# Performance work log

Measured on AMD Instinct MI355X. Metric: run time of the kernel, lower is better.

The kernel has to match this reference:

```python
import jax, jax.numpy as jnp
import numpy as np

L, D, H, F = 6, 1024, 8, 2048
B, S, IN = 4, 2048, 128
DK = D // H
EPS = 1e-6


def layer_norm(x, s, b):
    mu = jnp.mean(x, -1, keepdims=True)
    var = jnp.mean((x - mu) ** 2, -1, keepdims=True)
    return (x - mu) * jax.lax.rsqrt(var + EPS) * s + b


def rotate_every_two(x):
    x1 = x[..., ::2]
    x2 = x[..., 1::2]
    return jnp.stack([-x2, x1], axis=-1).reshape(x.shape)


def rotary_tables():
    # torchscale RetNet xpos-style angles: each freq repeated twice (interleaved)
    angle = 1.0 / (10000.0 ** jnp.linspace(0.0, 1.0, DK // 2))
    angle = jnp.repeat(angle, 2)                      # [DK]
    idx = jnp.arange(S, dtype=jnp.float32)[:, None]   # [S,1]
    return jnp.sin(idx * angle), jnp.cos(idx * angle)  # [S,DK] each


def decay_mask():
    # gamma_h = 1 - 2^(-5-h); D[h,n,m] = gamma_h^(n-m) for n>=m else 0,
    # row-normalized by sqrt(row sum) as in torchscale.
    gamma = 1.0 - 2.0 ** (-5.0 - jnp.arange(H, dtype=jnp.float32))  # [H]
    n = jnp.arange(S)
    diff = jnp.clip(n[:, None] - n[None, :], 0)                      # [S,S]
    tril = n[:, None] >= n[None, :]
    m = jnp.where(tril[None], gamma[:, None, None] ** diff[None].astype(jnp.float32), 0.0)
    return m / jnp.sqrt(jnp.sum(m, -1, keepdims=True))               # [H,S,S]


def setup_inputs() -> dict:
    key = jax.random.key(0)
    ks = iter(jax.random.split(key, 24))
    p = lambda shape: jax.random.normal(next(ks), shape, jnp.float32) * 0.02
    return {
        "x": jax.random.normal(next(ks), (B, S, IN), jnp.float32),
        "W_in": p((IN, D)), "b_in": jnp.zeros((D,), jnp.float32),
        "Wq": p((L, D, D)), "Wk": p((L, D, D)), "Wv": p((L, D, D)),
        "Wg": p((L, D, D)), "Wo": p((L, D, D)),
        "gn_g": jnp.ones((L, D), jnp.float32),
        "ln1_s": jnp.ones((L, D), jnp.float32), "ln1_b": jnp.zeros((L, D), jnp.float32),
        "ffn_W1": p((L, D, F)), "ffn_b1": jnp.zeros((L, F), jnp.float32),
        "ffn_W2": p((L, F, D)), "ffn_b2": jnp.zeros((L, D), jnp.float32),
        "ln2_s": jnp.ones((L, D), jnp.float32), "ln2_b": jnp.zeros((L, D), jnp.float32),
        "lnf_s": jnp.ones((D,), jnp.float32), "lnf_b": jnp.zeros((D,), jnp.float32),
        "W_reg": p((D, 1)), "b_reg": jnp.zeros((1,), jnp.float32),
    }


def reference(x, W_in, b_in, Wq, Wk, Wv, Wg, Wo, gn_g, ln1_s, ln1_b,
              ffn_W1, ffn_b1, ffn_W2, ffn_b2, ln2_s, ln2_b, lnf_s, lnf_b,
              W_reg, b_reg):
    sin, cos = rotary_tables()
    dmask = decay_mask()  # [H,S,S]
    h = x @ W_in + b_in   # input_embed
    for l in range(L):
        # --- multi-scale retention (pre-norm) ---
        y = layer_norm(h, ln1_s[l], ln1_b[l])
        q = (y @ Wq[l]).reshape(B, S, H, DK).transpose(0, 2, 1, 3)
        k = (y @ Wk[l]).reshape(B, S, H, DK).transpose(0, 2, 1, 3) * (DK ** -0.5)
        v = (y @ Wv[l]).reshape(B, S, H, DK).transpose(0, 2, 1, 3)
        q = q * cos + rotate_every_two(q) * sin
        k = k * cos + rotate_every_two(k) * sin
        scores = jnp.einsum('bhnd,bhmd->bhnm', q, k)
        ret = scores * dmask[None]
        ret = ret / jnp.clip(jnp.abs(ret).sum(-1, keepdims=True), 1.0, None)
        o = jnp.einsum('bhnm,bhmd->bhnd', ret, v)
        # per-head group (RMS) norm
        o = o * jax.lax.rsqrt(jnp.mean(o * o, -1, keepdims=True) + EPS)
        o = o.transpose(0, 2, 1, 3).reshape(B, S, D) * gn_g[l]
        g = y @ Wg[l]
        h = h + (jax.nn.silu(g) * o) @ Wo[l]
        # --- FFN (pre-norm) ---
        y = layer_norm(h, ln2_s[l], ln2_b[l])
        h = h + jax.nn.gelu(y @ ffn_W1[l] + ffn_b1[l]) @ ffn_W2[l] + ffn_b2[l]
    h = layer_norm(h, lnf_s, lnf_b)
    out = 1.1 * jax.nn.sigmoid(h @ W_reg + b_reg) - 0.05
    return out.squeeze(-1)  # [B,S]
```

## Files before the change

### kernel.cpp

```cpp
#include <hip/hip_runtime.h>

#define L_ 6
#define D_ 1024
#define H_ 8
#define F_ 2048
#define B_ 4
#define S_ 2048
#define IN_ 128
#define DK_ 128
#define BS_ (B_*S_)
#define D2_ 4096

typedef short bf16x8 __attribute__((ext_vector_type(8)));
typedef float f32x4 __attribute__((ext_vector_type(4)));

__device__ inline float b2f(unsigned short u){ union{unsigned int i; float f;} v; v.i = ((unsigned int)u)<<16; return v.f; }
__device__ inline unsigned short f2b(float f){ union{unsigned int i; float f;} v; v.f = f; unsigned int r = v.i + 0x7FFFu + ((v.i>>16)&1u); return (unsigned short)(r>>16); }
__device__ inline unsigned int cvtpk(float lo, float hi){
    unsigned int r; asm("v_cvt_pk_bf16_f32 %0, %1, %2" : "=v"(r) : "v"(lo), "v"(hi)); return r;
}

__device__ inline void gld16(const void* g, void* l) {
    __builtin_amdgcn_global_load_lds((const __attribute__((address_space(1))) unsigned int*)g,
                                     (__attribute__((address_space(3))) unsigned int*)l, 16, 0, 0);
}

#define GBAR() do{ asm volatile("" ::: "memory"); __builtin_amdgcn_s_barrier(); asm volatile("" ::: "memory"); }while(0)

__global__ void f32_to_bf16_k(const float* __restrict__ in, unsigned short* __restrict__ out, int n)
{
    int i = blockIdx.x*256 + threadIdx.x;
    if (i < n) out[i] = f2b(in[i]);
}

__global__ void transpose_w_k(const float* __restrict__ in, unsigned short* __restrict__ out, int R, int C, size_t ostride)
{
    __shared__ float tile[32][33];
    int z = blockIdx.z;
    const float* pi = in + (size_t)z*R*C;
    unsigned short* po = out + (size_t)z*ostride;
    int c0 = blockIdx.x*32, r0 = blockIdx.y*32;
    int tx = threadIdx.x, ty = threadIdx.y;
    #pragma unroll
    for (int i=0;i<4;i++) tile[ty+i*8][tx] = pi[(size_t)(r0+ty+i*8)*C + c0+tx];
    __syncthreads();
    #pragma unroll
    for (int i=0;i<4;i++) po[(size_t)(c0+ty+i*8)*R + r0+tx] = f2b(tile[tx][ty+i*8]);
}

__global__ void transpose_v_k(const unsigned short* __restrict__ vb, unsigned short* __restrict__ vT)
{
    __shared__ unsigned short tile[32][33];
    int z = blockIdx.z;
    int b = z >> 3, hh = z & 7;
    int s0 = blockIdx.x*32, d0 = blockIdx.y*32;
    int tx = threadIdx.x, ty = threadIdx.y;
    #pragma unroll
    for (int i=0;i<4;i++) tile[ty+i*8][tx] = vb[(size_t)(b*S_ + s0+ty+i*8)*D2_ + hh*DK_ + d0+tx];
    __syncthreads();
    #pragma unroll
    for (int i=0;i<4;i++) vT[((size_t)z*DK_ + d0+ty+i*8)*S_ + s0+tx] = tile[tx][ty+i*8];
}

__global__ void build_sincos_k(float* __restrict__ cost, float* __restrict__ sint)
{
    int id = blockIdx.x*256 + threadIdx.x;
    int s = id >> 6, i = id & 63;
    float ang = powf(10000.f, -(float)i/63.f);
    float a = (float)s * ang;
    float sv = sinf(a), cv = cosf(a);
    sint[s*DK_ + 2*i] = sv; sint[s*DK_ + 2*i+1] = sv;
    cost[s*DK_ + 2*i] = cv; cost[s*DK_ + 2*i+1] = cv;
}

__global__ void build_dnorm_k(float* __restrict__ dnorm)
{
    int id = blockIdx.x*256 + threadIdx.x;
    int h = id >> 11, n = id & (S_-1);
    double g = 1.0 - exp2((double)(-5 - h));
    double sum = (1.0 - exp(((double)(n+1))*log(g))) / (1.0 - g);
    dnorm[id] = (float)(1.0/sqrt(sum));
}

__device__ inline float bsum(float v, float* red, int t)
{
    #pragma unroll
    for (int m=32; m; m>>=1) v += __shfl_xor(v, m);
    __syncthreads();
    if ((t & 63) == 0) red[t>>6] = v;
    __syncthreads();
    return red[0]+red[1]+red[2]+red[3];
}

__global__ __launch_bounds__(256) void ln_to_bf16_k(const float* __restrict__ x, const float* __restrict__ s,
                                                    const float* __restrict__ b, unsigned short* __restrict__ y)
{
    __shared__ float red[4];
    int row = blockIdx.x, t = threadIdx.x;
    const float* xr = x + (size_t)row * D_;
    float4 v = ((const float4*)xr)[t];
    float mu = bsum(v.x+v.y+v.z+v.w, red, t) * (1.f/D_);
    float d0=v.x-mu, d1=v.y-mu, d2=v.z-mu, d3=v.w-mu;
    float var = bsum(d0*d0+d1*d1+d2*d2+d3*d3, red, t) * (1.f/D_);
    float inv = rsqrtf(var + 1e-6f);
    int c = t*4;
    float o0 = d0*inv*s[c+0] + b[c+0];
    float o1 = d1*inv*s[c+1] + b[c+1];
    float o2 = d2*inv*s[c+2] + b[c+2];
    float o3 = d3*inv*s[c+3] + b[c+3];
    unsigned long long pk = (unsigned long long)f2b(o0) | ((unsigned long long)f2b(o1)<<16)
                          | ((unsigned long long)f2b(o2)<<32) | ((unsigned long long)f2b(o3)<<48);
    *(unsigned long long*)(y + (size_t)row*D_ + c) = pk;
}

template<int MODE, int BN>
__global__ __launch_bounds__(512, 2)
void gemm6(const unsigned short* __restrict__ A,
           const unsigned short* __restrict__ Bt,
           const float* __restrict__ bias,
           void* __restrict__ Cv,
           int M, int N, int K)
{
    constexpr int BM   = 256;
    constexpr int IR   = 8;
    constexpr int JR   = BN/64;
    constexpr int ASUB = BM*64;
    constexpr int BSUB = BN*64;
    constexpr int BUFSZ= 2*ASUB + 2*BSUB;
    constexpr int AP   = 2;
    constexpr int BP   = BN/128;
    __shared__ unsigned char lds[2*BUFSZ];

    const int tid = threadIdx.x, lane = tid & 63, w = tid >> 6;
    const int r16 = lane & 15, quad = (lane >> 4) & 3;
    const int wm = w >> 2, wn = w & 3;

    const int nwg = (int)(gridDim.x * gridDim.y);
    int bid = (int)(blockIdx.y * gridDim.x + blockIdx.x);
    if ((nwg & 7) == 0) bid = (bid & 7) * (nwg >> 3) + (bid >> 3);
    const int m0 = (bid / (int)gridDim.x) * BM;
    const int n0 = (bid % (int)gridDim.x) * BN;

    const int srow = tid >> 2;
    const int schk = (tid & 3) ^ ((tid >> 3) & 3);
    const unsigned short* gA = A  + (size_t)(m0 + srow) * K + schk*8;
    const unsigned short* gB = Bt + (size_t)(n0 + srow) * K + schk*8;

    const int rchk = (quad ^ ((r16 >> 1) & 3)) * 16;
    const int aoff = (wm*128 + r16)*64 + rchk;
    const int boff = (wn*(BN/4) + r16)*64 + rchk;

    f32x4 acc[IR][JR];
    #pragma unroll
    for (int i=0;i<IR;i++)
      #pragma unroll
      for (int j=0;j<JR;j++) acc[i][j] = (f32x4){0.f,0.f,0.f,0.f};

    const int NT = K >> 6;

    auto stageA = [&](int t, int kk){
        unsigned char* dst = lds + (t&1)*BUFSZ + kk*ASUB;
        const unsigned short* src = gA + (size_t)t*64 + kk*32;
        #pragma unroll
        for (int p=0;p<AP;p++)
            gld16(src + (size_t)(p*128)*K, dst + p*8192 + tid*16);
    };
    auto stageB = [&](int t, int kk){
        unsigned char* dst = lds + (t&1)*BUFSZ + 2*ASUB + kk*BSUB;
        const unsigned short* src = gB + (size_t)t*64 + kk*32;
        #pragma unroll
        for (int p=0;p<BP;p++)
            gld16(src + (size_t)(p*128)*K, dst + p*8192 + tid*16);
    };

    stageA(0,0); stageB(0,0); stageA(0,1); stageB(0,1);
    if constexpr (BN==256) asm volatile("s_waitcnt vmcnt(4)" ::: "memory");
    else                   asm volatile("s_waitcnt vmcnt(3)" ::: "memory");
    GBAR();

    for (int t = 0; t < NT; ++t) {
        const unsigned char* cb = lds + (t&1)*BUFSZ;
        const bool pre = (t+1 < NT);
        #pragma unroll
        for (int kk = 0; kk < 2; ++kk) {
            const unsigned char* ak = cb + kk*ASUB;
            const unsigned char* bk = cb + 2*ASUB + kk*BSUB;
            if constexpr (BN == 256) {
                bf16x8 af[4], bg[JR];
                #pragma unroll
                for (int i=0;i<4;i++) af[i] = *(const bf16x8*)(ak + aoff + i*1024);
                #pragma unroll
                for (int j=0;j<JR;j++) bg[j] = *(const bf16x8*)(bk + boff + j*1024);
                if (pre) stageA(t+1, kk);
                GBAR();
                asm volatile("s_waitcnt lgkmcnt(0)" ::: "memory");
                __builtin_amdgcn_s_setprio(1);
                #pragma unroll
                for (int i=0;i<4;i++)
                  #pragma unroll
                  for (int j=0;j<JR;j++)
                    acc[i][j] = __builtin_amdgcn_mfma_f32_16x16x32_bf16(af[i], bg[j], acc[i][j], 0,0,0);
                __builtin_amdgcn_s_setprio(0);
                GBAR();
                #pragma unroll
                for (int i=0;i<4;i++) af[i] = *(const bf16x8*)(ak + aoff + (4+i)*1024);
                if (pre) stageB(t+1, kk);
                GBAR();
                asm volatile("s_waitcnt lgkmcnt(0)" ::: "memory");
                __builtin_amdgcn_s_setprio(1);
                #pragma unroll
                for (int i=0;i<4;i++)
                  #pragma unroll
                  for (int j=0;j<JR;j++)
                    acc[4+i][j] = __builtin_amdgcn_mfma_f32_16x16x32_bf16(af[i], bg[j], acc[4+i][j], 0,0,0);
                __builtin_amdgcn_s_setprio(0);
                if (pre) asm volatile("s_waitcnt vmcnt(4)" ::: "memory");
                else     asm volatile("s_waitcnt vmcnt(0)" ::: "memory");
                GBAR();
            } else {
                bf16x8 af[8], bg[JR];
                #pragma unroll
                for (int i=0;i<8;i++) af[i] = *(const bf16x8*)(ak + aoff + i*1024);
                #pragma unroll
                for (int j=0;j<JR;j++) bg[j] = *(const bf16x8*)(bk + boff + j*1024);
                if (pre) { stageA(t+1, kk); stageB(t+1, kk); }
                GBAR();
                asm volatile("s_waitcnt lgkmcnt(0)" ::: "memory");
                __builtin_amdgcn_s_setprio(1);
                #pragma unroll
                for (int i=0;i<8;i++)
                  #pragma unroll
                  for (int j=0;j<JR;j++)
                    acc[i][j] = __builtin_amdgcn_mfma_f32_16x16x32_bf16(af[i], bg[j], acc[i][j], 0,0,0);
                __builtin_amdgcn_s_setprio(0);
                if (pre) asm volatile("s_waitcnt vmcnt(3)" ::: "memory");
                else     asm volatile("s_waitcnt vmcnt(0)" ::: "memory");
                GBAR();
            }
        }
    }

    float* Cf = (float*)Cv;
    unsigned short* Cb = (unsigned short*)Cv;
    float bvs[JR];
    #pragma unroll
    for (int j=0;j<JR;j++) bvs[j] = bias ? bias[n0 + wn*(BN/4) + j*16 + r16] : 0.f;
    #pragma unroll
    for (int i=0;i<IR;i++) {
      #pragma unroll
      for (int r=0;r<4;r++) {
        const size_t crow = (size_t)(m0 + wm*128 + i*16 + quad*4 + r);
        #pragma unroll
        for (int j=0;j<JR;j++) {
          const int ccol = n0 + wn*(BN/4) + j*16 + r16;
          float v = acc[i][j][r];
          if (MODE == 0) { Cf[crow*N + ccol] = v + bvs[j]; }
          else if (MODE == 1) { Cf[crow*N + ccol] += v + bvs[j]; }
          else if (MODE == 2) { Cb[crow*N + ccol] = f2b(v); }
          else {
            v += bvs[j];
            float t3 = tanhf(0.7978845608028654f*(v + 0.044715f*v*v*v));
            Cb[crow*N + ccol] = f2b(0.5f*v*(1.f + t3));
          }
        }
      }
    }
}

__global__ __launch_bounds__(256) void rope_qk_k(unsigned short* __restrict__ qkvg,
                                                 const float* __restrict__ cost, const float* __restrict__ sint)
{
    int id = blockIdx.x*256 + threadIdx.x;
    int row = id >> 9;
    int d = (id & 511) * 2;
    int s = row & (S_-1);
    int dk = d & (DK_-1);
    float c0 = cost[s*DK_ + dk],   s0 = sint[s*DK_ + dk];
    float c1 = cost[s*DK_ + dk+1], s1 = sint[s*DK_ + dk+1];
    size_t off = (size_t)row*D2_ + d;
    unsigned int qu = *(unsigned int*)(qkvg + off);
    float q0 = b2f((unsigned short)(qu & 0xffffu)), q1 = b2f((unsigned short)(qu >> 16));
    float r0 = q0*c0 - q1*s0;
    float r1 = q1*c1 + q0*s1;
    *(unsigned int*)(qkvg + off) = (unsigned int)f2b(r0) | ((unsigned int)f2b(r1) << 16);
    const float sc = 0.08838834764831845f;
    unsigned int ku = *(unsigned int*)(qkvg + off + 1024);
    float k0 = b2f((unsigned short)(ku & 0xffffu))*sc, k1 = b2f((unsigned short)(ku >> 16))*sc;
    float t0 = k0*c0 - k1*s0;
    float t1 = k1*c1 + k0*s1;
    *(unsigned int*)(qkvg + off + 1024) = (unsigned int)f2b(t0) | ((unsigned int)f2b(t1) << 16);
}

__global__ __launch_bounds__(256, 2) void retention_k(const unsigned short* __restrict__ qk_base,
    const unsigned short* __restrict__ vT, const float* __restrict__ dnorm,
    const float* __restrict__ gng, unsigned short* __restrict__ attnin)
{
    __shared__ __align__(16) unsigned char lds[75776];
    const int pr = blockIdx.x;
    const int bh = blockIdx.y;
    const int b = bh >> 3, hh = bh & 7;
    const int tid = threadIdx.x, lane = tid & 63, w = tid >> 6;
    const int r16 = lane & 15, quad = lane >> 4;

    const float l2g = log2f(1.f - exp2f(-5.f - (float)hh));
    const int ithr = (int)(45.f / (-l2g));
    const unsigned int mkr = (r16 & 7) << 4;

    const int mk2  = ((tid >> 4) & 7) << 4;
    const int mkv2 = ((tid >> 3) & 7) << 4;
    const unsigned short* ksrc = qk_base + 1024 + ((size_t)(b*S_) + (tid>>4))*D2_ + hh*DK_
                                + ((((tid&15)*16) ^ mk2) >> 1);
    const unsigned short* vsrc = vT + ((size_t)bh*DK_ + (tid>>3))*S_ + ((((tid&7)*16) ^ mkv2) >> 1);

    float Aarr[4];
    #pragma unroll
    for (int r=0;r<4;r++) Aarr[r] = exp2f(l2g * (float)(63 - (w*16 + quad*4 + r)));

    float* dsums = (float*)(lds + 73728);
    float* ssums = (float*)(lds + 74752);

    auto stage = [&](int c2, int kt2){
        const unsigned short* s0 = ksrc + (size_t)kt2*64*D2_;
        #pragma unroll
        for (int i=0;i<4;i++)
            gld16(s0 + (size_t)i*16*D2_, lds + c2*16384 + i*4096 + w*1024);
        const unsigned short* s1 = vsrc + kt2*64;
        #pragma unroll
        for (int j=0;j<4;j++)
            gld16(s1 + (size_t)j*32*S_, lds + 32768 + c2*16384 + j*4096 + w*1024);
    };

    int cur = 0;

    #pragma unroll 1
    for (int seg = 0; seg < 2; ++seg) {
        const int qt = seg ? pr : (31 - pr);
        const int n0 = qt * 64;
        const int kt_start = max(0, (n0 - ithr) >> 6);

        bf16x8 qf[4][4];
        const unsigned short* qptr = qk_base + ((size_t)(b*S_ + n0 + r16))*D2_ + hh*DK_;
        #pragma unroll
        for (int qtl=0;qtl<4;qtl++)
          #pragma unroll
          for (int c=0;c<4;c++) qf[qtl][c] = *(const bf16x8*)(qptr + qtl*16*D2_ + c*32 + quad*8);

        f32x4 oacc[4][2];
        #pragma unroll
        for (int qtl=0;qtl<4;qtl++)
          #pragma unroll
          for (int dt=0;dt<2;dt++) oacc[qtl][dt] = (f32x4){0.f,0.f,0.f,0.f};
        float dsum[4] = {0.f,0.f,0.f,0.f};

        stage(cur, kt_start);

        #pragma unroll 1
        for (int kt = kt_start; kt <= qt; ++kt) {
            if (kt < qt) { stage(cur^1, kt+1); asm volatile("s_waitcnt vmcnt(8)" ::: "memory"); }
            else         { asm volatile("s_waitcnt vmcnt(0)" ::: "memory"); }
            GBAR();

            const unsigned char* kb = lds + cur*16384;
            bf16x8 kf[4];
            #pragma unroll
            for (int c=0;c<4;c++)
                kf[c] = *(const bf16x8*)(kb + (w*16 + r16)*256 + ((c*64 + quad*16) ^ mkr));
            f32x4 sf[4];
            #pragma unroll
            for (int qtl=0;qtl<4;qtl++) sf[qtl] = (f32x4){0.f,0.f,0.f,0.f};
            __builtin_amdgcn_s_setprio(1);
            #pragma unroll
            for (int c=0;c<4;c++)
              #pragma unroll
              for (int qtl=0;qtl<4;qtl++)
                sf[qtl] = __builtin_amdgcn_mfma_f32_16x16x32_bf16(kf[c], qf[qtl][c], sf[qtl], 0,0,0);
            __builtin_amdgcn_s_setprio(0);

            const bool diag = (kt == qt);
            #pragma unroll
            for (int qtl=0;qtl<4;qtl++) {
                float Bq = exp2f(l2g * (float)(n0 + qtl*16 + r16 - kt*64 - 63));
                float pv[4];
                #pragma unroll
                for (int r=0;r<4;r++) {
                    float p = sf[qtl][r] * Aarr[r] * Bq;
                    if (diag && (w*16 + quad*4 + r > qtl*16 + r16)) p = 0.f;
                    dsum[qtl] += fabsf(p);
                    pv[r] = p;
                }
                unsigned long long pk = (unsigned long long)cvtpk(pv[0], pv[1])
                                      | ((unsigned long long)cvtpk(pv[2], pv[3]) << 32);
                *(unsigned long long*)(lds + 65536 + (qtl*16 + r16)*128 + ((w*32 + quad*8) ^ mkr)) = pk;
            }
            asm volatile("s_waitcnt lgkmcnt(0)" ::: "memory");
            GBAR();

            const unsigned char* vb = lds + 32768 + cur*16384;
            bf16x8 pa[4][2], vf[2][2];
            #pragma unroll
            for (int qtl=0;qtl<4;qtl++)
              #pragma unroll
              for (int ks=0;ks<2;ks++)
                pa[qtl][ks] = *(const bf16x8*)(lds + 65536 + (qtl*16 + r16)*128 + ((ks*64 + quad*16) ^ mkr));
            #pragma unroll
            for (int dt=0;dt<2;dt++)
              #pragma unroll
              for (int ks=0;ks<2;ks++)
                vf[dt][ks] = *(const bf16x8*)(vb + (w*32 + dt*16 + r16)*128 + ((ks*64 + quad*16) ^ mkr));
            __builtin_amdgcn_s_setprio(1);
            #pragma unroll
            for (int qtl=0;qtl<4;qtl++)
              #pragma unroll
              for (int dt=0;dt<2;dt++)
                #pragma unroll
                for (int ks=0;ks<2;ks++)
                  oacc[qtl][dt] = __builtin_amdgcn_mfma_f32_16x16x32_bf16(pa[qtl][ks], vf[dt][ks], oacc[qtl][dt], 0,0,0);
            __builtin_amdgcn_s_setprio(0);
            GBAR();
            cur ^= 1;
        }

        #pragma unroll
        for (int qtl=0;qtl<4;qtl++) {
            float dv = dsum[qtl];
            dv += __shfl_xor(dv, 16); dv += __shfl_xor(dv, 32);
            if (lane < 16) dsums[w*64 + qtl*16 + r16] = dv;
        }
        __syncthreads();
        float scl[4][4], pss[4][4];
        #pragma unroll
        for (int qtl=0;qtl<4;qtl++) {
            #pragma unroll
            for (int r=0;r<4;r++) {
                int nl = qtl*16 + quad*4 + r;
                float dv = dsums[nl] + dsums[64+nl] + dsums[128+nl] + dsums[192+nl];
                float nr = dnorm[hh*S_ + n0 + nl];
                float sc = nr / fmaxf(1.f, dv * nr);
                scl[qtl][r] = sc;
                float s2 = 0.f;
                #pragma unroll
                for (int dt=0;dt<2;dt++) { float t = oacc[qtl][dt][r]*sc; s2 += t*t; }
                s2 += __shfl_xor(s2,1); s2 += __shfl_xor(s2,2);
                s2 += __shfl_xor(s2,4); s2 += __shfl_xor(s2,8);
                pss[qtl][r] = s2;
            }
        }
        if (r16 == 0) {
            #pragma unroll
            for (int qtl=0;qtl<4;qtl++)
              #pragma unroll
              for (int r=0;r<4;r++)
                ssums[w*64 + qtl*16 + quad*4 + r] = pss[qtl][r];
        }
        __syncthreads();
        #pragma unroll
        for (int qtl=0;qtl<4;qtl++) {
            float rms[4];
            #pragma unroll
            for (int r=0;r<4;r++) {
                int nl = qtl*16 + quad*4 + r;
                float s2 = ssums[nl] + ssums[64+nl] + ssums[128+nl] + ssums[192+nl];
                rms[r] = rsqrtf(s2*(1.f/DK_) + 1e-6f);
            }
            #pragma unroll
            for (int dt=0;dt<2;dt++) {
                int d = w*32 + dt*16 + r16;
                float gg = gng[hh*DK_ + d];
                #pragma unroll
                for (int r=0;r<4;r++) {
                    int n = n0 + qtl*16 + quad*4 + r;
                    float gv = b2f(qk_base[(size_t)(b*S_ + n)*D2_ + 3072 + hh*DK_ + d]);
                    float sg = gv / (1.f + expf(-gv));
                    float ov = oacc[qtl][dt][r]*scl[qtl][r]*rms[r]*gg;
                    attnin[(size_t)(b*S_ + n)*D_ + hh*DK_ + d] = f2b(ov*sg);
                }
            }
        }
        __syncthreads();
    }
}

__global__ __launch_bounds__(256) void head_out_k(const float* __restrict__ h, const float* __restrict__ s,
    const float* __restrict__ b, const float* __restrict__ wreg, const float* __restrict__ breg,
    float* __restrict__ out)
{
    __shared__ float red[4];
    int row = blockIdx.x, t = threadIdx.x;
    const float* xr = h + (size_t)row*D_;
    float4 v = ((const float4*)xr)[t];
    float mu = bsum(v.x+v.y+v.z+v.w, red, t) * (1.f/D_);
    float d0=v.x-mu, d1=v.y-mu, d2=v.z-mu, d3=v.w-mu;
    float var = bsum(d0*d0+d1*d1+d2*d2+d3*d3, red, t) * (1.f/D_);
    float inv = rsqrtf(var + 1e-6f);
    int c = t*4;
    float dot = (d0*inv*s[c+0]+b[c+0])*wreg[c+0] + (d1*inv*s[c+1]+b[c+1])*wreg[c+1]
              + (d2*inv*s[c+2]+b[c+2])*wreg[c+2] + (d3*inv*s[c+3]+b[c+3])*wreg[c+3];
    dot = bsum(dot, red, t);
    if (t == 0) out[row] = 1.1f / (1.f + expf(-(dot + breg[0]))) - 0.05f;
}

extern "C" void kernel_launch(void* const* d_in, const int* in_sizes, int n_in,
                              void* d_out, int out_size, void* d_ws, size_t ws_size,
                              hipStream_t stream)
{
    (void)in_sizes; (void)n_in; (void)out_size; (void)ws_size;
    const float* x    = (const float*)d_in[0];
    const float* W_in = (const float*)d_in[1];
    const float* b_in = (const float*)d_in[2];
    const float* Wq   = (const float*)d_in[3];
    const float* Wk   = (const float*)d_in[4];
    const float* Wv   = (const float*)d_in[5];
    const float* Wg   = (const float*)d_in[6];
    const float* Wo   = (const float*)d_in[7];
    const float* gn_g = (const float*)d_in[8];
    const float* ln1s = (const float*)d_in[9];
    const float* ln1b = (const float*)d_in[10];
    const float* W1   = (const float*)d_in[11];
    const float* b1   = (const float*)d_in[12];
    const float* W2   = (const float*)d_in[13];
    const float* b2   = (const float*)d_in[14];
    const float* ln2s = (const float*)d_in[15];
    const float* ln2b = (const float*)d_in[16];
    const float* lnfs = (const float*)d_in[17];
    const float* lnfb = (const float*)d_in[18];
    const float* Wreg = (const float*)d_in[19];
    const float* breg = (const float*)d_in[20];

    char* ws = (char*)d_ws;
    size_t off = 0;
    auto alloc = [&](size_t bytes) { char* p = ws + off; off += (bytes + 255) & ~(size_t)255; return p; };

    const size_t DD = (size_t)D_*D_;
    unsigned short* wqkvgT = (unsigned short*)alloc((size_t)L_*4*DD*2);
    unsigned short* woT  = (unsigned short*)alloc((size_t)L_*DD*2);
    unsigned short* w1T  = (unsigned short*)alloc((size_t)L_*D_*F_*2);
    unsigned short* w2T  = (unsigned short*)alloc((size_t)L_*D_*F_*2);
    unsigned short* winT = (unsigned short*)alloc((size_t)D_*IN_*2);
    unsigned short* x_bf = (unsigned short*)alloc((size_t)BS_*IN_*2);
    float*          hbuf = (float*)alloc((size_t)BS_*D_*4);
    unsigned short* y_bf = (unsigned short*)alloc((size_t)BS_*D_*2);
    unsigned short* qkvg = (unsigned short*)alloc((size_t)BS_*D2_*2);
    unsigned short* vTb  = (unsigned short*)alloc((size_t)BS_*D_*2);
    float*          cost = (float*)alloc((size_t)S_*DK_*4);
    float*          sint = (float*)alloc((size_t)S_*DK_*4);
    float*          dnrm = (float*)alloc((size_t)H_*S_*4);
    unsigned short* attn = y_bf;
    unsigned short* midb = qkvg;

    dim3 tb(32, 8);

    f32_to_bf16_k<<<(BS_*IN_)/256, 256, 0, stream>>>(x, x_bf, BS_*IN_);
    transpose_w_k<<<dim3(32,32,L_), tb, 0, stream>>>(Wq, wqkvgT + 0*DD, D_, D_, 4*DD);
    transpose_w_k<<<dim3(32,32,L_), tb, 0, stream>>>(Wk, wqkvgT + 1*DD, D_, D_, 4*DD);
    transpose_w_k<<<dim3(32,32,L_), tb, 0, stream>>>(Wv, wqkvgT + 2*DD, D_, D_, 4*DD);
    transpose_w_k<<<dim3(32,32,L_), tb, 0, stream>>>(Wg, wqkvgT + 3*DD, D_, D_, 4*DD);
    transpose_w_k<<<dim3(32,32,L_), tb, 0, stream>>>(Wo, woT, D_, D_, DD);
    transpose_w_k<<<dim3(64,32,L_), tb, 0, stream>>>(W1, w1T, D_, F_, (size_t)D_*F_);
    transpose_w_k<<<dim3(32,64,L_), tb, 0, stream>>>(W2, w2T, F_, D_, (size_t)D_*F_);
    transpose_w_k<<<dim3(32, 4, 1), tb, 0, stream>>>(W_in, winT, IN_, D_, (size_t)D_*IN_);
    build_sincos_k<<<(S_*64)/256, 256, 0, stream>>>(cost, sint);
    build_dnorm_k<<<(H_*S_)/256, 256, 0, stream>>>(dnrm);

    gemm6<0,128><<<dim3(D_/128, BS_/256), 512, 0, stream>>>(x_bf, winT, b_in, hbuf, BS_, D_, IN_);

    for (int l = 0; l < L_; ++l) {
        ln_to_bf16_k<<<BS_, 256, 0, stream>>>(hbuf, ln1s + l*D_, ln1b + l*D_, y_bf);
        gemm6<2,256><<<dim3(D2_/256, BS_/256), 512, 0, stream>>>(y_bf, wqkvgT + (size_t)l*4*DD, nullptr, qkvg, BS_, D2_, D_);
        rope_qk_k<<<(BS_*D_/2)/256, 256, 0, stream>>>(qkvg, cost, sint);
        transpose_v_k<<<dim3(S_/32, DK_/32, B_*H_), tb, 0, stream>>>(qkvg + 2048, vTb);
        retention_k<<<dim3(16, B_*H_), 256, 0, stream>>>(qkvg, vTb, dnrm, gn_g + l*D_, attn);
        gemm6<1,128><<<dim3(D_/128, BS_/256), 512, 0, stream>>>(attn, woT + (size_t)l*DD, nullptr, hbuf, BS_, D_, D_);
        ln_to_bf16_k<<<BS_, 256, 0, stream>>>(hbuf, ln2s + l*D_, ln2b + l*D_, y_bf);
        gemm6<3,256><<<dim3(F_/256, BS_/256), 512, 0, stream>>>(y_bf, w1T + (size_t)l*D_*F_, b1 + l*F_, midb, BS_, F_, D_);
        gemm6<1,128><<<dim3(D_/128, BS_/256), 512, 0, stream>>>(midb, w2T + (size_t)l*D_*F_, b2 + l*D_, hbuf, BS_, D_, F_);
    }

    head_out_k<<<BS_, 256, 0, stream>>>(hbuf, lnfs, lnfb, Wreg, breg, (float*)d_out);
}
```

Measured before the change: 2.022 ms.

## Fuse RoPE into QKVG GEMM epilogue and remap retention block order

Removes the separate rope_qk_k pass by applying the rotary embedding and the k scaling inside the QKVG GEMM epilogue. Pair partners are fetched with a lane shuffle, and sin/cos values are read from the tables per output element. This saves one read-modify-write pass over the q and k halves of the QKVG buffer per layer. Separately, the retention kernel's block index is remapped so that consecutive blocks interleave (batch, head) pairs, which likely aims at better load balance or cache locality across the differing decay lengths. The risk is more epilogue cost in the GEMM: a divergent branch and extra table loads.

```diff
diff --git a/kernel.cpp b/kernel.cpp
--- a/kernel.cpp
+++ b/kernel.cpp
@@ -119,7 +119,8 @@
            const unsigned short* __restrict__ Bt,
            const float* __restrict__ bias,
            void* __restrict__ Cv,
-           int M, int N, int K)
+           int M, int N, int K,
+           const float* __restrict__ ctab, const float* __restrict__ stab)
 {
     constexpr int BM   = 256;
     constexpr int IR   = 8;
@@ -257,6 +258,18 @@
           if (MODE == 0) { Cf[crow*N + ccol] = v + bvs[j]; }
           else if (MODE == 1) { Cf[crow*N + ccol] += v + bvs[j]; }
           else if (MODE == 2) { Cb[crow*N + ccol] = f2b(v); }
+          else if (MODE == 4) {
+            if (ccol < 2048) {
+                int srw = (int)(crow & (S_-1));
+                int dk = ccol & (DK_-1);
+                float cv = ctab[srw*DK_ + dk], sv = stab[srw*DK_ + dk];
+                float sc = (ccol < 1024) ? 1.f : 0.08838834764831845f;
+                float vs = v * sc;
+                float vp = __shfl_xor(vs, 1);
+                v = (r16 & 1) ? (vs*cv + vp*sv) : (vs*cv - vp*sv);
+            }
+            Cb[crow*N + ccol] = f2b(v);
+          }
           else {
             v += bvs[j];
             float t3 = tanhf(0.7978845608028654f*(v + 0.044715f*v*v*v));
@@ -267,37 +280,15 @@
     }
 }
 
-__global__ __launch_bounds__(256) void rope_qk_k(unsigned short* __restrict__ qkvg,
-                                                 const float* __restrict__ cost, const float* __restrict__ sint)
-{
-    int id = blockIdx.x*256 + threadIdx.x;
-    int row = id >> 9;
-    int d = (id & 511) * 2;
-    int s = row & (S_-1);
-    int dk = d & (DK_-1);
-    float c0 = cost[s*DK_ + dk],   s0 = sint[s*DK_ + dk];
-    float c1 = cost[s*DK_ + dk+1], s1 = sint[s*DK_ + dk+1];
-    size_t off = (size_t)row*D2_ + d;
-    unsigned int qu = *(unsigned int*)(qkvg + off);
-    float q0 = b2f((unsigned short)(qu & 0xffffu)), q1 = b2f((unsigned short)(qu >> 16));
-    float r0 = q0*c0 - q1*s0;
-    float r1 = q1*c1 + q0*s1;
-    *(unsigned int*)(qkvg + off) = (unsigned int)f2b(r0) | ((unsigned int)f2b(r1) << 16);
-    const float sc = 0.08838834764831845f;
-    unsigned int ku = *(unsigned int*)(qkvg + off + 1024);
-    float k0 = b2f((unsigned short)(ku & 0xffffu))*sc, k1 = b2f((unsigned short)(ku >> 16))*sc;
-    float t0 = k0*c0 - k1*s0;
-    float t1 = k1*c1 + k0*s1;
-    *(unsigned int*)(qkvg + off + 1024) = (unsigned int)f2b(t0) | ((unsigned int)f2b(t1) << 16);
-}
-
 __global__ __launch_bounds__(256, 2) void retention_k(const unsigned short* __restrict__ qk_base,
     const unsigned short* __restrict__ vT, const float* __restrict__ dnorm,
     const float* __restrict__ gng, unsigned short* __restrict__ attnin)
 {
     __shared__ __align__(16) unsigned char lds[75776];
-    const int pr = blockIdx.x;
-    const int bh = blockIdx.y;
+    const int Lf = (int)(blockIdx.y * gridDim.x + blockIdx.x);
+    const int kx = Lf & 7, mm = Lf >> 3;
+    const int bh = 4*kx + (mm >> 4);
+    const int pr = mm & 15;
     const int b = bh >> 3, hh = bh & 7;
     const int tid = threadIdx.x, lane = tid & 63, w = tid >> 6;
     const int r16 = lane & 15, quad = lane >> 4;
@@ -561,18 +552,17 @@
     build_sincos_k<<<(S_*64)/256, 256, 0, stream>>>(cost, sint);
     build_dnorm_k<<<(H_*S_)/256, 256, 0, stream>>>(dnrm);
 
-    gemm6<0,128><<<dim3(D_/128, BS_/256), 512, 0, stream>>>(x_bf, winT, b_in, hbuf, BS_, D_, IN_);
+    gemm6<0,128><<<dim3(D_/128, BS_/256), 512, 0, stream>>>(x_bf, winT, b_in, hbuf, BS_, D_, IN_, nullptr, nullptr);
 
     for (int l = 0; l < L_; ++l) {
         ln_to_bf16_k<<<BS_, 256, 0, stream>>>(hbuf, ln1s + l*D_, ln1b + l*D_, y_bf);
-        gemm6<2,256><<<dim3(D2_/256, BS_/256), 512, 0, stream>>>(y_bf, wqkvgT + (size_t)l*4*DD, nullptr, qkvg, BS_, D2_, D_);
-        rope_qk_k<<<(BS_*D_/2)/256, 256, 0, stream>>>(qkvg, cost, sint);
+        gemm6<4,256><<<dim3(D2_/256, BS_/256), 512, 0, stream>>>(y_bf, wqkvgT + (size_t)l*4*DD, nullptr, qkvg, BS_, D2_, D_, cost, sint);
         transpose_v_k<<<dim3(S_/32, DK_/32, B_*H_), tb, 0, stream>>>(qkvg + 2048, vTb);
         retention_k<<<dim3(16, B_*H_), 256, 0, stream>>>(qkvg, vTb, dnrm, gn_g + l*D_, attn);
-        gemm6<1,128><<<dim3(D_/128, BS_/256), 512, 0, stream>>>(attn, woT + (size_t)l*DD, nullptr, hbuf, BS_, D_, D_);
+        gemm6<1,128><<<dim3(D_/128, BS_/256), 512, 0, stream>>>(attn, woT + (size_t)l*DD, nullptr, hbuf, BS_, D_, D_, nullptr, nullptr);
         ln_to_bf16_k<<<BS_, 256, 0, stream>>>(hbuf, ln2s + l*D_, ln2b + l*D_, y_bf);
-        gemm6<3,256><<<dim3(F_/256, BS_/256), 512, 0, stream>>>(y_bf, w1T + (size_t)l*D_*F_, b1 + l*F_, midb, BS_, F_, D_);
-        gemm6<1,128><<<dim3(D_/128, BS_/256), 512, 0, stream>>>(midb, w2T + (size_t)l*D_*F_, b2 + l*D_, hbuf, BS_, D_, F_);
+        gemm6<3,256><<<dim3(F_/256, BS_/256), 512, 0, stream>>>(y_bf, w1T + (size_t)l*D_*F_, b1 + l*F_, midb, BS_, F_, D_, nullptr, nullptr);
+        gemm6<1,128><<<dim3(D_/128, BS_/256), 512, 0, stream>>>(midb, w2T + (size_t)l*D_*F_, b2 + l*D_, hbuf, BS_, D_, F_, nullptr, nullptr);
     }
 
     head_out_k<<<BS_, 256, 0, stream>>>(hbuf, lnfs, lnfb, Wreg, breg, (float*)d_out);
```

Result: slower. 2.153 ms (+6.5%).
